# Optimization experiments

Measured on AMD Instinct MI355X. Metric: run time of the kernel, lower is better.

Reference implementation:

```python
import jax, jax.numpy as jnp
import numpy as np

NNZ = 16384
OUT_F = 1024
IN_F = 1024


def setup_inputs() -> dict:
    key = jax.random.key(0)
    k1, k2, k3, k4 = jax.random.split(key, 4)
    x = jax.random.normal(k1, (8, 4096, IN_F), dtype=jnp.float32)
    base_weight = (jax.random.normal(k2, (OUT_F, IN_F), dtype=jnp.float32) * 0.02).astype(jnp.float16)
    ortho_values = (jax.random.normal(k3, (NNZ,), dtype=jnp.float32) * 0.02).astype(jnp.float16)
    # unique flat indices (row * in_features + col), matching load_from_weights
    ortho_indices = jax.random.permutation(k4, OUT_F * IN_F)[:NNZ].astype(jnp.int32)
    alpha = jnp.ones((), dtype=jnp.float32)
    return {"x": x, "base_weight": base_weight, "ortho_values": ortho_values,
            "ortho_indices": ortho_indices, "alpha": alpha}


def reference(x, base_weight, ortho_values, ortho_indices, alpha):
    # Y = X @ W_base^T + alpha * (X @ W_ortho^T)  (torch F.linear convention)
    out_f, in_f = base_weight.shape
    lead = x.shape[:-1]
    xf = x.reshape(-1, in_f)  # [tokens, in]
    base_out = xf @ base_weight.astype(jnp.float32).T  # fp16 weight upcast, as in forward

    rows = ortho_indices // in_f
    cols = ortho_indices % in_f
    ortho_matrix = jnp.zeros((out_f, in_f), dtype=jnp.float32).at[rows, cols].set(
        ortho_values.astype(jnp.float32))
    ortho_out = xf @ ortho_matrix.T

    output = base_out + alpha.astype(jnp.float32) * ortho_out
    return output.reshape(*lead, out_f)
```

## Files before the change

kernel.cpp:

```cpp
#include <hip/hip_runtime.h>

#define IN_F 1024
#define OUT_F 1024
#define NNZ 16384

typedef _Float16 f16;
typedef _Float16 f16x4 __attribute__((ext_vector_type(4)));
typedef _Float16 f16x8 __attribute__((ext_vector_type(8)));
typedef float f32x4 __attribute__((ext_vector_type(4)));
typedef unsigned short ushort8 __attribute__((ext_vector_type(8)));

#define AS1 __attribute__((address_space(1)))
#define AS3 __attribute__((address_space(3)))


__device__ __forceinline__ int compute_mode(const unsigned short* __restrict__ w,
                                            float* smax, int* semax) {
  int t = threadIdx.x;
  const float* wf = (const float*)w;
  float m32 = fmaxf(fabsf(wf[t]), fabsf(wf[t + 256]));
  int e8 = 0;
#pragma unroll
  for (int j = 0; j < 8; ++j) {
    unsigned short u = w[t * 8 + j];
    int e = (u >> 7) & 0xFF;
    e8 = e > e8 ? e : e8;
  }
  smax[t] = m32; semax[t] = e8;
  __syncthreads();
  for (int s = 128; s > 0; s >>= 1) {
    if (t < s) {
      smax[t] = fmaxf(smax[t], smax[t + s]);
      semax[t] = semax[t] > semax[t + s] ? semax[t] : semax[t + s];
    }
    __syncthreads();
  }
  int m;
  if (!(smax[0] > 1e-6f)) m = 2;
  else if (semax[0] >= 140) m = 0;
  else m = 1;
  return m;
}

__device__ __forceinline__ float load_w(const void* base, size_t i, int mode) {
  if (mode == 0) return ((const float*)base)[i];
  if (mode == 1) {
    unsigned int u = (unsigned int)((const unsigned short*)base)[i] << 16;
    return __uint_as_float(u);
  }
  return (float)((const f16*)base)[i];
}

__global__ void prep_base(const void* __restrict__ base, f16* __restrict__ Wl) {
  __shared__ float smax[256];
  __shared__ int semax[256];
  int mode = compute_mode((const unsigned short*)base, smax, semax);
  int id = blockIdx.x * 256 + threadIdx.x;
  size_t off = (size_t)id * 8;
  f16x8 h;
  if (mode == 0) {
    const float* b = (const float*)base + off;
    float4 v0 = *reinterpret_cast<const float4*>(b);
    float4 v1 = *reinterpret_cast<const float4*>(b + 4);
    h = (f16x8){(f16)v0.x, (f16)v0.y, (f16)v0.z, (f16)v0.w,
                (f16)v1.x, (f16)v1.y, (f16)v1.z, (f16)v1.w};
  } else if (mode == 1) {
    ushort8 uv = *reinterpret_cast<const ushort8*>((const unsigned short*)base + off);
#pragma unroll
    for (int j = 0; j < 8; ++j)
      h[j] = (f16)__uint_as_float((unsigned int)uv[j] << 16);
  } else {
    h = *reinterpret_cast<const f16x8*>((const f16*)base + off);
  }
  *reinterpret_cast<f16x8*>(Wl + off) = h;
}

__global__ void prep_scatter(const void* __restrict__ base,
                             const void* __restrict__ vals,
                             const int* __restrict__ idx,
                             const float* __restrict__ alpha,
                             f16* __restrict__ Wl) {
  __shared__ float smax[256];
  __shared__ int semax[256];
  int mode = compute_mode((const unsigned short*)base, smax, semax);
  int i = blockIdx.x * 256 + threadIdx.x;
  if (i >= NNZ) return;
  int id = idx[i];
  float v = load_w(base, id, mode) + alpha[0] * load_w(vals, i, mode);
  Wl[id] = (f16)v;
}

__global__ void __launch_bounds__(256) conv_x(const float* __restrict__ X,
                                              f16* __restrict__ Xs, int total) {
  int stride = gridDim.x * 256;
  for (int id = blockIdx.x * 256 + threadIdx.x; id < total; id += stride) {
    size_t off = (size_t)id * 8;
    const float* p = X + off;
    float4 v0 = *reinterpret_cast<const float4*>(p);
    float4 v1 = *reinterpret_cast<const float4*>(p + 4);
    f16x8 h = {(f16)v0.x, (f16)v0.y, (f16)v0.z, (f16)v0.w,
               (f16)v1.x, (f16)v1.y, (f16)v1.z, (f16)v1.w};
    *reinterpret_cast<f16x8*>(Xs + off) = h;
  }
}

#define SB0 __builtin_amdgcn_sched_barrier(0)
#define VMW(N) asm volatile("s_waitcnt vmcnt(" #N ")" ::: "memory")


#define ISSUE_QA11(QI, KT1, AP)                                                \
    __builtin_amdgcn_global_load_lds(                                          \
        (const AS1 void*)(Xs + rowOffA[QI] + (KT1) * 64 + swzc),               \
        (AS3 void*)(&sA[((AP) * 4 + (QI)) * 4096 + t * 8]), 16, 0, 0)

#define ISSUE_QB11(QI, KT1, BP)                                                \
    __builtin_amdgcn_global_load_lds(                                          \
        (const AS1 void*)(Wl + rowOffB[QI] + (KT1) * 64 + swzc),               \
        (AS3 void*)(&sB[((BP) * 4 + (QI)) * 4096 + t * 8]), 16, 0, 0)

#define DSREAD11(AP, BP, S_) do {                                              \
    _Pragma("unroll")                                                          \
    for (int qq_ = 0; qq_ < 2; ++qq_) {                                        \
      int qa_ = ((AP) * 4 + wm * 2 + qq_) * 4096;                              \
      _Pragma("unroll")                                                        \
      for (int mf_ = 0; mf_ < 4; ++mf_) {                                      \
        int r_ = mf_ * 16 + lr;                                                \
        int blk_ = ((S_) * 4 + lk) ^ (lr & 7);                                 \
        afr[qq_][mf_] = *reinterpret_cast<const f16x8*>(&sA[qa_ + r_ * 64 + blk_ * 8]); \
      }                                                                        \
    }                                                                          \
    int qb_ = ((BP) * 4 + wn) * 4096;                                          \
    _Pragma("unroll")                                                          \
    for (int nf_ = 0; nf_ < 4; ++nf_) {                                        \
      int r_ = nf_ * 16 + lr;                                                  \
      int blk_ = ((S_) * 4 + lk) ^ (lr & 7);                                   \
      bfr[nf_] = *reinterpret_cast<const f16x8*>(&sB[qb_ + r_ * 64 + blk_ * 8]); \
    }                                                                          \
  } while (0)

#define MFMA32_FREE do {                                                       \
    __builtin_amdgcn_s_setprio(1);                                             \
    _Pragma("unroll")                                                          \
    for (int qq_ = 0; qq_ < 2; ++qq_)                                          \
      _Pragma("unroll")                                                        \
      for (int mf_ = 0; mf_ < 4; ++mf_)                                        \
        _Pragma("unroll")                                                      \
        for (int nf_ = 0; nf_ < 4; ++nf_)                                      \
          acc[qq_ * 4 + mf_][nf_] = __builtin_amdgcn_mfma_f32_16x16x32_f16(    \
              afr[qq_][mf_], bfr[nf_], acc[qq_ * 4 + mf_][nf_], 0, 0, 0);      \
    __builtin_amdgcn_s_setprio(0);                                             \
  } while (0)

#define KTILE12(AP, BP, KT, ISSB, ISSA, VMN, LASTBAR) do {                     \
    DSREAD11(AP, BP, 0);                                                       \
    if (ISSB) {                                                                \
      ISSUE_QB11(0, (KT) + 1, ((KT) + 1) & 1); ISSUE_QB11(1, (KT) + 1, ((KT) + 1) & 1); \
      ISSUE_QB11(2, (KT) + 1, ((KT) + 1) & 1); ISSUE_QB11(3, (KT) + 1, ((KT) + 1) & 1); } \
    MFMA32_FREE;                                                               \
    DSREAD11(AP, BP, 1);                                                       \
    if (ISSA) {                                                                \
      ISSUE_QA11(0, (KT) + 2, ((KT) + 2) % 3); ISSUE_QA11(1, (KT) + 2, ((KT) + 2) % 3); \
      ISSUE_QA11(2, (KT) + 2, ((KT) + 2) % 3); ISSUE_QA11(3, (KT) + 2, ((KT) + 2) % 3); } \
    MFMA32_FREE;                                                               \
    if (LASTBAR) {                                                             \
      VMW(VMN);                                                                \
      __builtin_amdgcn_s_barrier();             \
      SB0;                              \
    }                                                                          \
  } while (0)

__global__ void __launch_bounds__(512, 2) gemm12(const f16* __restrict__ Xs,
                                                 const f16* __restrict__ Wl,
                                                 float* __restrict__ C) {
  extern __shared__ f16 lds[];
  f16* sA = lds;
  f16* sB = lds + 49152;

  int bidx = blockIdx.x;
  int q = gridDim.x >> 3;
  int wg = (bidx & 7) * q + (bidx >> 3);
  int mt = wg >> 2, nt = wg & 3;

  int t = threadIdx.x;
  int lane = t & 63;
  int w = t >> 6;
  int wm = w >> 2;
  int wn = w & 3;
  int lr = lane & 15;
  int lk = lane >> 4;

  int rS = t >> 3;
  int swzc = (((t & 7) ^ (rS & 7)) << 3);
  size_t rowOffA[4], rowOffB[4];
#pragma unroll
  for (int qi = 0; qi < 4; ++qi) {
    rowOffA[qi] = (size_t)(mt * 256 + qi * 64 + rS) * IN_F;
    rowOffB[qi] = (size_t)(nt * 256 + qi * 64 + rS) * IN_F;
  }

  f16x8 afr[2][4], bfr[4];
  f32x4 acc[8][4];
#pragma unroll
  for (int i = 0; i < 8; ++i)
#pragma unroll
    for (int j = 0; j < 4; ++j)
      acc[i][j] = (f32x4){0.f, 0.f, 0.f, 0.f};

  ISSUE_QA11(0, 0, 0); ISSUE_QA11(1, 0, 0); ISSUE_QA11(2, 0, 0); ISSUE_QA11(3, 0, 0);
  ISSUE_QB11(0, 0, 0); ISSUE_QB11(1, 0, 0); ISSUE_QB11(2, 0, 0); ISSUE_QB11(3, 0, 0);
  ISSUE_QA11(0, 1, 1); ISSUE_QA11(1, 1, 1); ISSUE_QA11(2, 1, 1); ISSUE_QA11(3, 1, 1);
  VMW(4);
  __builtin_amdgcn_s_barrier();
  SB0;

  KTILE12(0, 0,  0, true,  true,  4, true);
  KTILE12(1, 1,  1, true,  true,  4, true);
  KTILE12(2, 0,  2, true,  true,  4, true);
  KTILE12(0, 1,  3, true,  true,  4, true);
  KTILE12(1, 0,  4, true,  true,  4, true);
  KTILE12(2, 1,  5, true,  true,  4, true);
  KTILE12(0, 0,  6, true,  true,  4, true);
  KTILE12(1, 1,  7, true,  true,  4, true);
  KTILE12(2, 0,  8, true,  true,  4, true);
  KTILE12(0, 1,  9, true,  true,  4, true);
  KTILE12(1, 0, 10, true,  true,  4, true);
  KTILE12(2, 1, 11, true,  true,  4, true);
  KTILE12(0, 0, 12, true,  true,  4, true);
  KTILE12(1, 1, 13, true,  true,  4, true);
  KTILE12(2, 0, 14, true,  false, 0, true);
  KTILE12(0, 1, 15, false, false, 0, false);

  float* Cw = C + (size_t)(mt * 256 + wm * 128 + lk * 4) * OUT_F + nt * 256 + wn * 64 + lr;
#pragma unroll
  for (int m = 0; m < 8; ++m) {
    int rowo = (m >> 2) * 64 + (m & 3) * 16;
#pragma unroll
    for (int nf = 0; nf < 4; ++nf)
#pragma unroll
      for (int g = 0; g < 4; ++g)
        Cw[(size_t)(rowo + g) * OUT_F + nf * 16] = acc[m][nf][g];
  }
}


#define MFMA32_PIN do {                                                        \
    asm volatile("s_waitcnt lgkmcnt(0)" ::: "memory");                         \
    SB0;                                                                       \
    __builtin_amdgcn_s_setprio(1);                                             \
    _Pragma("unroll")                                                          \
    for (int qq_ = 0; qq_ < 2; ++qq_)                                          \
      _Pragma("unroll")                                                        \
      for (int mf_ = 0; mf_ < 4; ++mf_)                                        \
        _Pragma("unroll")                                                      \
        for (int nf_ = 0; nf_ < 4; ++nf_)                                      \
          acc[qq_ * 4 + mf_][nf_] = __builtin_amdgcn_mfma_f32_16x16x32_f16(    \
              afr[qq_][mf_], bfr[nf_], acc[qq_ * 4 + mf_][nf_], 0, 0, 0);      \
    __builtin_amdgcn_s_setprio(0);                                             \
  } while (0)

#define KTILE11(AP, BP, KT, ISSB, ISSA, VMN, LASTBAR) do {                     \
    DSREAD11(AP, BP, 0);                                                       \
    if (ISSB) { SB0;                                                           \
      ISSUE_QB11(0, (KT) + 1, ((KT) + 1) & 1); ISSUE_QB11(1, (KT) + 1, ((KT) + 1) & 1); \
      ISSUE_QB11(2, (KT) + 1, ((KT) + 1) & 1); ISSUE_QB11(3, (KT) + 1, ((KT) + 1) & 1); } \
    MFMA32_PIN;                                                                \
    DSREAD11(AP, BP, 1);                                                       \
    if (ISSA) { SB0;                                                           \
      ISSUE_QA11(0, (KT) + 2, ((KT) + 2) % 3); ISSUE_QA11(1, (KT) + 2, ((KT) + 2) % 3); \
      ISSUE_QA11(2, (KT) + 2, ((KT) + 2) % 3); ISSUE_QA11(3, (KT) + 2, ((KT) + 2) % 3); } \
    MFMA32_PIN;                                                                \
    if (LASTBAR) {                                                             \
      SB0; VMW(VMN); SB0;                                                      \
      __builtin_amdgcn_s_barrier();                                            \
      SB0;                                                                     \
    }                                                                          \
  } while (0)

__global__ void __launch_bounds__(512, 2) gemm11(const f16* __restrict__ Xs,
                                                 const f16* __restrict__ Wl,
                                                 float* __restrict__ C) {
  extern __shared__ f16 lds[];
  f16* sA = lds;
  f16* sB = lds + 49152;

  int bidx = blockIdx.x;
  int q = gridDim.x >> 3;
  int wg = (bidx & 7) * q + (bidx >> 3);
  int mt = wg >> 2, nt = wg & 3;

  int t = threadIdx.x;
  int lane = t & 63;
  int w = t >> 6;
  int wm = w >> 2;
  int wn = w & 3;
  int lr = lane & 15;
  int lk = lane >> 4;

  int rS = t >> 3;
  int swzc = (((t & 7) ^ (rS & 7)) << 3);
  size_t rowOffA[4], rowOffB[4];
#pragma unroll
  for (int qi = 0; qi < 4; ++qi) {
    rowOffA[qi] = (size_t)(mt * 256 + qi * 64 + rS) * IN_F;
    rowOffB[qi] = (size_t)(nt * 256 + qi * 64 + rS) * IN_F;
  }

  f16x8 afr[2][4], bfr[4];
  f32x4 acc[8][4];
#pragma unroll
  for (int i = 0; i < 8; ++i)
#pragma unroll
    for (int j = 0; j < 4; ++j)
      acc[i][j] = (f32x4){0.f, 0.f, 0.f, 0.f};

  ISSUE_QA11(0, 0, 0); ISSUE_QA11(1, 0, 0); ISSUE_QA11(2, 0, 0); ISSUE_QA11(3, 0, 0);
  ISSUE_QB11(0, 0, 0); ISSUE_QB11(1, 0, 0); ISSUE_QB11(2, 0, 0); ISSUE_QB11(3, 0, 0);
  ISSUE_QA11(0, 1, 1); ISSUE_QA11(1, 1, 1); ISSUE_QA11(2, 1, 1); ISSUE_QA11(3, 1, 1);
  SB0; VMW(4); SB0;
  __builtin_amdgcn_s_barrier();
  SB0;

  KTILE11(0, 0,  0, true,  true,  4, true);
  KTILE11(1, 1,  1, true,  true,  4, true);
  KTILE11(2, 0,  2, true,  true,  4, true);
  KTILE11(0, 1,  3, true,  true,  4, true);
  KTILE11(1, 0,  4, true,  true,  4, true);
  KTILE11(2, 1,  5, true,  true,  4, true);
  KTILE11(0, 0,  6, true,  true,  4, true);
  KTILE11(1, 1,  7, true,  true,  4, true);
  KTILE11(2, 0,  8, true,  true,  4, true);
  KTILE11(0, 1,  9, true,  true,  4, true);
  KTILE11(1, 0, 10, true,  true,  4, true);
  KTILE11(2, 1, 11, true,  true,  4, true);
  KTILE11(0, 0, 12, true,  true,  4, true);
  KTILE11(1, 1, 13, true,  true,  4, true);
  KTILE11(2, 0, 14, true,  false, 0, true);
  KTILE11(0, 1, 15, false, false, 0, false);

  float* Cw = C + (size_t)(mt * 256 + wm * 128 + lk * 4) * OUT_F + nt * 256 + wn * 64 + lr;
#pragma unroll
  for (int m = 0; m < 8; ++m) {
    int rowo = (m >> 2) * 64 + (m & 3) * 16;
#pragma unroll
    for (int nf = 0; nf < 4; ++nf)
#pragma unroll
      for (int g = 0; g < 4; ++g)
        Cw[(size_t)(rowo + g) * OUT_F + nf * 16] = acc[m][nf][g];
  }
}

extern "C" void kernel_launch(void* const* d_in, const int* in_sizes, int n_in,
                              void* d_out, int out_size, void* d_ws, size_t ws_size,
                              hipStream_t stream) {
  const float* X = (const float*)d_in[0];
  const void* base = d_in[1];
  const void* vals = d_in[2];
  const int* idx = (const int*)d_in[3];
  const float* alpha = (const float*)d_in[4];
  float* out = (float*)d_out;
  f16* Wl = (f16*)d_ws;
  f16* Xs = (f16*)((char*)d_ws + 2 * 1024 * 1024 + 4096);

  int M = in_sizes[0] / IN_F;
  int total = (M * IN_F) / 8;

  prep_base<<<dim3(512), dim3(256), 0, stream>>>(base, Wl);
  prep_scatter<<<dim3((NNZ + 255) / 256), dim3(256), 0, stream>>>(base, vals, idx, alpha, Wl);
  conv_x<<<dim3(2048), dim3(256), 0, stream>>>(X, Xs, total);

  hipError_t e = hipFuncSetAttribute(reinterpret_cast<const void*>(&gemm12),
                                     hipFuncAttributeMaxDynamicSharedMemorySize, 163840);
  if (e == hipSuccess) {
    gemm12<<<dim3((M / 256) * 4), dim3(512), 163840, stream>>>(Xs, Wl, out);
  } else {
    (void)hipFuncSetAttribute(reinterpret_cast<const void*>(&gemm11),
                              hipFuncAttributeMaxDynamicSharedMemorySize, 163840);
    gemm11<<<dim3((M / 256) * 4), dim3(512), 163840, stream>>>(Xs, Wl, out);
  }
}
```

Baseline: 121.7 us.

## Switch GEMM to 128x128 tiles with 256 threads and fuse scatter into conv_x

Adds a new gemm13 kernel that uses 128x128 output tiles, 4 waves and half the LDS (80KB), launching four times as many workgroups. It keeps the same triple-buffered A and double-buffered B global_load_lds pipeline. The sparse scatter is also folded into the conv_x kernel, run by its first 64 blocks, which removes one launch. Smaller tiles give more blocks and better occupancy, but each tile reuses loaded data less and needs more global/L2 traffic. The scatter writing Wl inside conv_x, before gemm, stays ordered because it writes only Wl and runs after prep_base.

```diff
diff --git a/kernel.cpp b/kernel.cpp
--- a/kernel.cpp
+++ b/kernel.cpp
@@ -5,7 +5,6 @@
 #define NNZ 16384
 
 typedef _Float16 f16;
-typedef _Float16 f16x4 __attribute__((ext_vector_type(4)));
 typedef _Float16 f16x8 __attribute__((ext_vector_type(8)));
 typedef float f32x4 __attribute__((ext_vector_type(4)));
 typedef unsigned short ushort8 __attribute__((ext_vector_type(8)));
@@ -75,23 +74,22 @@
   *reinterpret_cast<f16x8*>(Wl + off) = h;
 }
 
-__global__ void prep_scatter(const void* __restrict__ base,
-                             const void* __restrict__ vals,
-                             const int* __restrict__ idx,
-                             const float* __restrict__ alpha,
-                             f16* __restrict__ Wl) {
+__global__ void __launch_bounds__(256) conv_x(const float* __restrict__ X,
+                                              f16* __restrict__ Xs, int total,
+                                              const void* __restrict__ base,
+                                              const void* __restrict__ vals,
+                                              const int* __restrict__ idx,
+                                              const float* __restrict__ alpha,
+                                              f16* __restrict__ Wl) {
   __shared__ float smax[256];
   __shared__ int semax[256];
-  int mode = compute_mode((const unsigned short*)base, smax, semax);
-  int i = blockIdx.x * 256 + threadIdx.x;
-  if (i >= NNZ) return;
-  int id = idx[i];
-  float v = load_w(base, id, mode) + alpha[0] * load_w(vals, i, mode);
-  Wl[id] = (f16)v;
-}
-
-__global__ void __launch_bounds__(256) conv_x(const float* __restrict__ X,
-                                              f16* __restrict__ Xs, int total) {
+  if (blockIdx.x < 64) {
+    int mode = compute_mode((const unsigned short*)base, smax, semax);
+    int i = blockIdx.x * 256 + threadIdx.x;
+    int id = idx[i];
+    float v = load_w(base, id, mode) + alpha[0] * load_w(vals, i, mode);
+    Wl[id] = (f16)v;
+  }
   int stride = gridDim.x * 256;
   for (int id = blockIdx.x * 256 + threadIdx.x; id < total; id += stride) {
     size_t off = (size_t)id * 8;
@@ -106,6 +104,142 @@
 
 #define SB0 __builtin_amdgcn_sched_barrier(0)
 #define VMW(N) asm volatile("s_waitcnt vmcnt(" #N ")" ::: "memory")
+
+
+#define ISSUE_QA13(QI, KT1, AP) do {                                           \
+    __builtin_amdgcn_global_load_lds(                                          \
+        (const AS1 void*)(Xs + rowOffA[QI][0] + (KT1) * 64 + swzc),            \
+        (AS3 void*)(&sA[((AP) * 2 + (QI)) * 4096 + t * 8]), 16, 0, 0);         \
+    __builtin_amdgcn_global_load_lds(                                          \
+        (const AS1 void*)(Xs + rowOffA[QI][1] + (KT1) * 64 + swzc),            \
+        (AS3 void*)(&sA[((AP) * 2 + (QI)) * 4096 + t * 8 + 2048]), 16, 0, 0);  \
+  } while (0)
+
+#define ISSUE_QB13(QI, KT1, BP) do {                                           \
+    __builtin_amdgcn_global_load_lds(                                          \
+        (const AS1 void*)(Wl + rowOffB[QI][0] + (KT1) * 64 + swzc),            \
+        (AS3 void*)(&sB[((BP) * 2 + (QI)) * 4096 + t * 8]), 16, 0, 0);         \
+    __builtin_amdgcn_global_load_lds(                                          \
+        (const AS1 void*)(Wl + rowOffB[QI][1] + (KT1) * 64 + swzc),            \
+        (AS3 void*)(&sB[((BP) * 2 + (QI)) * 4096 + t * 8 + 2048]), 16, 0, 0);  \
+  } while (0)
+
+#define DSREAD13(AP, BP, S_) do {                                              \
+    int qa_ = ((AP) * 2 + wm) * 4096;                                          \
+    _Pragma("unroll")                                                          \
+    for (int mf_ = 0; mf_ < 4; ++mf_) {                                        \
+      int r_ = mf_ * 16 + lr;                                                  \
+      int blk_ = ((S_) * 4 + lk) ^ (lr & 7);                                   \
+      afr[mf_] = *reinterpret_cast<const f16x8*>(&sA[qa_ + r_ * 64 + blk_ * 8]); \
+    }                                                                          \
+    int qb_ = ((BP) * 2 + wn) * 4096;                                          \
+    _Pragma("unroll")                                                          \
+    for (int nf_ = 0; nf_ < 4; ++nf_) {                                        \
+      int r_ = nf_ * 16 + lr;                                                  \
+      int blk_ = ((S_) * 4 + lk) ^ (lr & 7);                                   \
+      bfr[nf_] = *reinterpret_cast<const f16x8*>(&sB[qb_ + r_ * 64 + blk_ * 8]); \
+    }                                                                          \
+  } while (0)
+
+#define MFMA16F do {                                                           \
+    __builtin_amdgcn_s_setprio(1);                                             \
+    _Pragma("unroll")                                                          \
+    for (int mf_ = 0; mf_ < 4; ++mf_)                                          \
+      _Pragma("unroll")                                                        \
+      for (int nf_ = 0; nf_ < 4; ++nf_)                                        \
+        acc[mf_][nf_] = __builtin_amdgcn_mfma_f32_16x16x32_f16(                \
+            afr[mf_], bfr[nf_], acc[mf_][nf_], 0, 0, 0);                       \
+    __builtin_amdgcn_s_setprio(0);                                             \
+  } while (0)
+
+#define KTILE13(AP, BP, KT, ISSB, ISSA, VMN, LASTBAR) do {                     \
+    DSREAD13(AP, BP, 0);                                                       \
+    if (ISSB) { ISSUE_QB13(0, (KT) + 1, ((KT) + 1) & 1);                       \
+                ISSUE_QB13(1, (KT) + 1, ((KT) + 1) & 1); }                     \
+    MFMA16F;                                                                   \
+    DSREAD13(AP, BP, 1);                                                       \
+    if (ISSA) { ISSUE_QA13(0, (KT) + 2, ((KT) + 2) % 3);                       \
+                ISSUE_QA13(1, (KT) + 2, ((KT) + 2) % 3); }                     \
+    MFMA16F;                                                                   \
+    if (LASTBAR) {                                                             \
+      VMW(VMN);                                                                \
+      __builtin_amdgcn_s_barrier();             \
+      SB0;                                                    \
+    }                                                                          \
+  } while (0)
+
+__global__ void __launch_bounds__(256, 2) gemm13(const f16* __restrict__ Xs,
+                                                 const f16* __restrict__ Wl,
+                                                 float* __restrict__ C) {
+  extern __shared__ f16 lds[];
+  f16* sA = lds;
+  f16* sB = lds + 24576;
+
+  int bidx = blockIdx.x;
+  int q = gridDim.x >> 3;
+  int wg = (bidx & 7) * q + (bidx >> 3);
+  int mt = wg >> 3, nt = wg & 7;
+
+  int t = threadIdx.x;
+  int lane = t & 63;
+  int w = t >> 6;
+  int wm = w >> 1;
+  int wn = w & 1;
+  int lr = lane & 15;
+  int lk = lane >> 4;
+
+  int rS = t >> 3;
+  int swzc = (((t & 7) ^ (rS & 7)) << 3);
+  size_t rowOffA[2][2], rowOffB[2][2];
+#pragma unroll
+  for (int qi = 0; qi < 2; ++qi)
+#pragma unroll
+    for (int h = 0; h < 2; ++h) {
+      rowOffA[qi][h] = (size_t)(mt * 128 + qi * 64 + h * 32 + rS) * IN_F;
+      rowOffB[qi][h] = (size_t)(nt * 128 + qi * 64 + h * 32 + rS) * IN_F;
+    }
+
+  f16x8 afr[4], bfr[4];
+  f32x4 acc[4][4];
+#pragma unroll
+  for (int i = 0; i < 4; ++i)
+#pragma unroll
+    for (int j = 0; j < 4; ++j)
+      acc[i][j] = (f32x4){0.f, 0.f, 0.f, 0.f};
+
+  ISSUE_QA13(0, 0, 0); ISSUE_QA13(1, 0, 0);
+  ISSUE_QB13(0, 0, 0); ISSUE_QB13(1, 0, 0);
+  ISSUE_QA13(0, 1, 1); ISSUE_QA13(1, 1, 1);
+  VMW(4);
+  __builtin_amdgcn_s_barrier();
+  SB0;
+
+  KTILE13(0, 0,  0, true,  true,  4, true);
+  KTILE13(1, 1,  1, true,  true,  4, true);
+  KTILE13(2, 0,  2, true,  true,  4, true);
+  KTILE13(0, 1,  3, true,  true,  4, true);
+  KTILE13(1, 0,  4, true,  true,  4, true);
+  KTILE13(2, 1,  5, true,  true,  4, true);
+  KTILE13(0, 0,  6, true,  true,  4, true);
+  KTILE13(1, 1,  7, true,  true,  4, true);
+  KTILE13(2, 0,  8, true,  true,  4, true);
+  KTILE13(0, 1,  9, true,  true,  4, true);
+  KTILE13(1, 0, 10, true,  true,  4, true);
+  KTILE13(2, 1, 11, true,  true,  4, true);
+  KTILE13(0, 0, 12, true,  true,  4, true);
+  KTILE13(1, 1, 13, true,  true,  4, true);
+  KTILE13(2, 0, 14, true,  false, 0, true);
+  KTILE13(0, 1, 15, false, false, 0, false);
+
+  float* Cw = C + (size_t)(mt * 128 + wm * 64 + lk * 4) * OUT_F + nt * 128 + wn * 64 + lr;
+#pragma unroll
+  for (int mf = 0; mf < 4; ++mf)
+#pragma unroll
+    for (int nf = 0; nf < 4; ++nf)
+#pragma unroll
+      for (int g = 0; g < 4; ++g)
+        Cw[(size_t)(mf * 16 + g) * OUT_F + nf * 16] = acc[mf][nf][g];
+}
 
 
 #define ISSUE_QA11(QI, KT1, AP)                                                \
@@ -164,8 +298,8 @@
     MFMA32_FREE;                                                               \
     if (LASTBAR) {                                                             \
       VMW(VMN);                                                                \
-      __builtin_amdgcn_s_barrier();             \
-      SB0;                              \
+      __builtin_amdgcn_s_barrier();                                            \
+      SB0;                                                                     \
     }                                                                          \
   } while (0)
 
@@ -242,113 +376,6 @@
   }
 }
 
-
-#define MFMA32_PIN do {                                                        \
-    asm volatile("s_waitcnt lgkmcnt(0)" ::: "memory");                         \
-    SB0;                                                                       \
-    __builtin_amdgcn_s_setprio(1);                                             \
-    _Pragma("unroll")                                                          \
-    for (int qq_ = 0; qq_ < 2; ++qq_)                                          \
-      _Pragma("unroll")                                                        \
-      for (int mf_ = 0; mf_ < 4; ++mf_)                                        \
-        _Pragma("unroll")                                                      \
-        for (int nf_ = 0; nf_ < 4; ++nf_)                                      \
-          acc[qq_ * 4 + mf_][nf_] = __builtin_amdgcn_mfma_f32_16x16x32_f16(    \
-              afr[qq_][mf_], bfr[nf_], acc[qq_ * 4 + mf_][nf_], 0, 0, 0);      \
-    __builtin_amdgcn_s_setprio(0);                                             \
-  } while (0)
-
-#define KTILE11(AP, BP, KT, ISSB, ISSA, VMN, LASTBAR) do {                     \
-    DSREAD11(AP, BP, 0);                                                       \
-    if (ISSB) { SB0;                                                           \
-      ISSUE_QB11(0, (KT) + 1, ((KT) + 1) & 1); ISSUE_QB11(1, (KT) + 1, ((KT) + 1) & 1); \
-      ISSUE_QB11(2, (KT) + 1, ((KT) + 1) & 1); ISSUE_QB11(3, (KT) + 1, ((KT) + 1) & 1); } \
-    MFMA32_PIN;                                                                \
-    DSREAD11(AP, BP, 1);                                                       \
-    if (ISSA) { SB0;                                                           \
-      ISSUE_QA11(0, (KT) + 2, ((KT) + 2) % 3); ISSUE_QA11(1, (KT) + 2, ((KT) + 2) % 3); \
-      ISSUE_QA11(2, (KT) + 2, ((KT) + 2) % 3); ISSUE_QA11(3, (KT) + 2, ((KT) + 2) % 3); } \
-    MFMA32_PIN;                                                                \
-    if (LASTBAR) {                                                             \
-      SB0; VMW(VMN); SB0;                                                      \
-      __builtin_amdgcn_s_barrier();                                            \
-      SB0;                                                                     \
-    }                                                                          \
-  } while (0)
-
-__global__ void __launch_bounds__(512, 2) gemm11(const f16* __restrict__ Xs,
-                                                 const f16* __restrict__ Wl,
-                                                 float* __restrict__ C) {
-  extern __shared__ f16 lds[];
-  f16* sA = lds;
-  f16* sB = lds + 49152;
-
-  int bidx = blockIdx.x;
-  int q = gridDim.x >> 3;
-  int wg = (bidx & 7) * q + (bidx >> 3);
-  int mt = wg >> 2, nt = wg & 3;
-
-  int t = threadIdx.x;
-  int lane = t & 63;
-  int w = t >> 6;
-  int wm = w >> 2;
-  int wn = w & 3;
-  int lr = lane & 15;
-  int lk = lane >> 4;
-
-  int rS = t >> 3;
-  int swzc = (((t & 7) ^ (rS & 7)) << 3);
-  size_t rowOffA[4], rowOffB[4];
-#pragma unroll
-  for (int qi = 0; qi < 4; ++qi) {
-    rowOffA[qi] = (size_t)(mt * 256 + qi * 64 + rS) * IN_F;
-    rowOffB[qi] = (size_t)(nt * 256 + qi * 64 + rS) * IN_F;
-  }
-
-  f16x8 afr[2][4], bfr[4];
-  f32x4 acc[8][4];
-#pragma unroll
-  for (int i = 0; i < 8; ++i)
-#pragma unroll
-    for (int j = 0; j < 4; ++j)
-      acc[i][j] = (f32x4){0.f, 0.f, 0.f, 0.f};
-
-  ISSUE_QA11(0, 0, 0); ISSUE_QA11(1, 0, 0); ISSUE_QA11(2, 0, 0); ISSUE_QA11(3, 0, 0);
-  ISSUE_QB11(0, 0, 0); ISSUE_QB11(1, 0, 0); ISSUE_QB11(2, 0, 0); ISSUE_QB11(3, 0, 0);
-  ISSUE_QA11(0, 1, 1); ISSUE_QA11(1, 1, 1); ISSUE_QA11(2, 1, 1); ISSUE_QA11(3, 1, 1);
-  SB0; VMW(4); SB0;
-  __builtin_amdgcn_s_barrier();
-  SB0;
-
-  KTILE11(0, 0,  0, true,  true,  4, true);
-  KTILE11(1, 1,  1, true,  true,  4, true);
-  KTILE11(2, 0,  2, true,  true,  4, true);
-  KTILE11(0, 1,  3, true,  true,  4, true);
-  KTILE11(1, 0,  4, true,  true,  4, true);
-  KTILE11(2, 1,  5, true,  true,  4, true);
-  KTILE11(0, 0,  6, true,  true,  4, true);
-  KTILE11(1, 1,  7, true,  true,  4, true);
-  KTILE11(2, 0,  8, true,  true,  4, true);
-  KTILE11(0, 1,  9, true,  true,  4, true);
-  KTILE11(1, 0, 10, true,  true,  4, true);
-  KTILE11(2, 1, 11, true,  true,  4, true);
-  KTILE11(0, 0, 12, true,  true,  4, true);
-  KTILE11(1, 1, 13, true,  true,  4, true);
-  KTILE11(2, 0, 14, true,  false, 0, true);
-  KTILE11(0, 1, 15, false, false, 0, false);
-
-  float* Cw = C + (size_t)(mt * 256 + wm * 128 + lk * 4) * OUT_F + nt * 256 + wn * 64 + lr;
-#pragma unroll
-  for (int m = 0; m < 8; ++m) {
-    int rowo = (m >> 2) * 64 + (m & 3) * 16;
-#pragma unroll
-    for (int nf = 0; nf < 4; ++nf)
-#pragma unroll
-      for (int g = 0; g < 4; ++g)
-        Cw[(size_t)(rowo + g) * OUT_F + nf * 16] = acc[m][nf][g];
-  }
-}
-
 extern "C" void kernel_launch(void* const* d_in, const int* in_sizes, int n_in,
                               void* d_out, int out_size, void* d_ws, size_t ws_size,
                               hipStream_t stream) {
@@ -365,16 +392,15 @@
   int total = (M * IN_F) / 8;
 
   prep_base<<<dim3(512), dim3(256), 0, stream>>>(base, Wl);
-  prep_scatter<<<dim3((NNZ + 255) / 256), dim3(256), 0, stream>>>(base, vals, idx, alpha, Wl);
-  conv_x<<<dim3(2048), dim3(256), 0, stream>>>(X, Xs, total);
-
-  hipError_t e = hipFuncSetAttribute(reinterpret_cast<const void*>(&gemm12),
-                                     hipFuncAttributeMaxDynamicSharedMemorySize, 163840);
+  conv_x<<<dim3(2048), dim3(256), 0, stream>>>(X, Xs, total, base, vals, idx, alpha, Wl);
+
+  hipError_t e = hipFuncSetAttribute(reinterpret_cast<const void*>(&gemm13),
+                                     hipFuncAttributeMaxDynamicSharedMemorySize, 81920);
   if (e == hipSuccess) {
+    gemm13<<<dim3((M / 128) * 8), dim3(256), 81920, stream>>>(Xs, Wl, out);
+  } else {
+    (void)hipFuncSetAttribute(reinterpret_cast<const void*>(&gemm12),
+                              hipFuncAttributeMaxDynamicSharedMemorySize, 163840);
     gemm12<<<dim3((M / 256) * 4), dim3(512), 163840, stream>>>(Xs, Wl, out);
-  } else {
-    (void)hipFuncSetAttribute(reinterpret_cast<const void*>(&gemm11),
-                              hipFuncAttributeMaxDynamicSharedMemorySize, 163840);
-    gemm11<<<dim3((M / 256) * 4), dim3(512), 163840, stream>>>(Xs, Wl, out);
-  }
-}
+  }
+}
```

Result: faster. 119.1 us (-2.1%).

## Fuse fp32-to-fp16 X conversion into GEMM by staging fp32 tiles in LDS

Applied to the files above, without the earlier changes.

The separate conv_x pass that converts X to fp16 is removed. A new gemm14 kernel streams fp32 X directly into LDS in half-width K tiles and converts to fp16 while building fragments. B tiles are reloaded every other step, with a reworked wait/barrier schedule. This avoids writing and re-reading a 64 MB fp16 copy of X, at the cost of twice the LDS traffic for A, per-fragment conversion ALU work, and twice as many barriers.

```diff
diff --git a/kernel.cpp b/kernel.cpp
--- a/kernel.cpp
+++ b/kernel.cpp
@@ -5,7 +5,6 @@
 #define NNZ 16384
 
 typedef _Float16 f16;
-typedef _Float16 f16x4 __attribute__((ext_vector_type(4)));
 typedef _Float16 f16x8 __attribute__((ext_vector_type(8)));
 typedef float f32x4 __attribute__((ext_vector_type(4)));
 typedef unsigned short ushort8 __attribute__((ext_vector_type(8)));
@@ -108,6 +107,169 @@
 #define VMW(N) asm volatile("s_waitcnt vmcnt(" #N ")" ::: "memory")
 
 
+#define ISSUE_A14(QI, KT1, AP)                                                 \
+    __builtin_amdgcn_global_load_lds(                                          \
+        (const AS1 void*)(X + rowOffA[QI] + (KT1) * 32 + swzcA),               \
+        (AS3 void*)(&sAf[((AP) * 4 + (QI)) * 2048 + t * 4]), 16, 0, 0)
+
+#define ISSUE_B14(QI, KTB1, BP)                                                \
+    __builtin_amdgcn_global_load_lds(                                          \
+        (const AS1 void*)(Wl + rowOffB[QI] + (KTB1) * 64 + swzc),              \
+        (AS3 void*)(&sB[((BP) * 4 + (QI)) * 4096 + t * 8]), 16, 0, 0)
+
+#define DSREAD_A14(AP) do {                                                    \
+    _Pragma("unroll")                                                          \
+    for (int qq_ = 0; qq_ < 2; ++qq_) {                                        \
+      int qa_ = ((AP) * 4 + wm * 2 + qq_) * 2048;                              \
+      _Pragma("unroll")                                                        \
+      for (int mf_ = 0; mf_ < 4; ++mf_) {                                      \
+        int r_ = mf_ * 16 + lr;                                                \
+        f32x4 a0_ = *reinterpret_cast<const f32x4*>(                           \
+            &sAf[qa_ + r_ * 32 + (((2 * lk) ^ (r_ & 7)) << 2)]);               \
+        f32x4 a1_ = *reinterpret_cast<const f32x4*>(                           \
+            &sAf[qa_ + r_ * 32 + (((2 * lk + 1) ^ (r_ & 7)) << 2)]);           \
+        afr[qq_][mf_] = (f16x8){(f16)a0_[0], (f16)a0_[1], (f16)a0_[2],         \
+                                (f16)a0_[3], (f16)a1_[0], (f16)a1_[1],         \
+                                (f16)a1_[2], (f16)a1_[3]};                     \
+      }                                                                        \
+    }                                                                          \
+  } while (0)
+
+#define DSREAD_B14(BP, S_) do {                                                \
+    int qb_ = ((BP) * 4 + wn) * 4096;                                          \
+    _Pragma("unroll")                                                          \
+    for (int nf_ = 0; nf_ < 4; ++nf_) {                                        \
+      int r_ = nf_ * 16 + lr;                                                  \
+      int blk_ = ((S_) * 4 + lk) ^ (lr & 7);                                   \
+      bfr[nf_] = *reinterpret_cast<const f16x8*>(&sB[qb_ + r_ * 64 + blk_ * 8]); \
+    }                                                                          \
+  } while (0)
+
+#define MFMA32_14 do {                                                         \
+    __builtin_amdgcn_s_setprio(1);                                             \
+    _Pragma("unroll")                                                          \
+    for (int qq_ = 0; qq_ < 2; ++qq_)                                          \
+      _Pragma("unroll")                                                        \
+      for (int mf_ = 0; mf_ < 4; ++mf_)                                        \
+        _Pragma("unroll")                                                      \
+        for (int nf_ = 0; nf_ < 4; ++nf_)                                      \
+          acc[qq_ * 4 + mf_][nf_] = __builtin_amdgcn_mfma_f32_16x16x32_f16(    \
+              afr[qq_][mf_], bfr[nf_], acc[qq_ * 4 + mf_][nf_], 0, 0, 0);      \
+    __builtin_amdgcn_s_setprio(0);                                             \
+  } while (0)
+
+#define KTILE14(AP, BP, S_, KT, ISSB, ISSA, VMN, GATE) do {                    \
+    DSREAD_A14(AP);                                                            \
+    DSREAD_B14(BP, S_);                                                        \
+    if (ISSB) {                                                                \
+      ISSUE_B14(0, ((KT) >> 1) + 1, (((KT) >> 1) + 1) & 1);                    \
+      ISSUE_B14(1, ((KT) >> 1) + 1, (((KT) >> 1) + 1) & 1);                    \
+      ISSUE_B14(2, ((KT) >> 1) + 1, (((KT) >> 1) + 1) & 1);                    \
+      ISSUE_B14(3, ((KT) >> 1) + 1, (((KT) >> 1) + 1) & 1); }                  \
+    MFMA32_14;                                                                 \
+    if (ISSA) {                                                                \
+      ISSUE_A14(0, (KT) + 2, ((KT) + 2) % 3);                                  \
+      ISSUE_A14(1, (KT) + 2, ((KT) + 2) % 3);                                  \
+      ISSUE_A14(2, (KT) + 2, ((KT) + 2) % 3);                                  \
+      ISSUE_A14(3, (KT) + 2, ((KT) + 2) % 3); }                                \
+    if (GATE) {                                                                \
+      VMW(VMN);                                                                \
+      __builtin_amdgcn_s_barrier();             \
+      SB0;                                                    \
+    }                                                                          \
+  } while (0)
+
+__global__ void __launch_bounds__(512, 2) gemm14(const float* __restrict__ X,
+                                                 const f16* __restrict__ Wl,
+                                                 float* __restrict__ C) {
+  extern __shared__ char lds[];
+  float* sAf = (float*)lds;
+  f16* sB = (f16*)(lds + 98304);
+
+  int bidx = blockIdx.x;
+  int q = gridDim.x >> 3;
+  int wg = (bidx & 7) * q + (bidx >> 3);
+  int mt = wg >> 2, nt = wg & 3;
+
+  int t = threadIdx.x;
+  int lane = t & 63;
+  int w = t >> 6;
+  int wm = w >> 2;
+  int wn = w & 3;
+  int lr = lane & 15;
+  int lk = lane >> 4;
+
+  int rS = t >> 3;
+  int swzc = (((t & 7) ^ (rS & 7)) << 3);
+  int swzcA = (((t & 7) ^ (rS & 7)) << 2);
+  size_t rowOffA[4], rowOffB[4];
+#pragma unroll
+  for (int qi = 0; qi < 4; ++qi) {
+    rowOffA[qi] = (size_t)(mt * 256 + qi * 64 + rS) * IN_F;
+    rowOffB[qi] = (size_t)(nt * 256 + qi * 64 + rS) * IN_F;
+  }
+
+  f16x8 afr[2][4], bfr[4];
+  f32x4 acc[8][4];
+#pragma unroll
+  for (int i = 0; i < 8; ++i)
+#pragma unroll
+    for (int j = 0; j < 4; ++j)
+      acc[i][j] = (f32x4){0.f, 0.f, 0.f, 0.f};
+
+  ISSUE_A14(0, 0, 0); ISSUE_A14(1, 0, 0); ISSUE_A14(2, 0, 0); ISSUE_A14(3, 0, 0);
+  ISSUE_B14(0, 0, 0); ISSUE_B14(1, 0, 0); ISSUE_B14(2, 0, 0); ISSUE_B14(3, 0, 0);
+  ISSUE_A14(0, 1, 1); ISSUE_A14(1, 1, 1); ISSUE_A14(2, 1, 1); ISSUE_A14(3, 1, 1);
+  VMW(4);
+  __builtin_amdgcn_s_barrier();
+  SB0;
+
+  KTILE14(0, 0, 0,  0, true,  true,  8, true);
+  KTILE14(1, 0, 1,  1, false, true,  4, true);
+  KTILE14(2, 1, 0,  2, true,  true,  8, true);
+  KTILE14(0, 1, 1,  3, false, true,  4, true);
+  KTILE14(1, 0, 0,  4, true,  true,  8, true);
+  KTILE14(2, 0, 1,  5, false, true,  4, true);
+  KTILE14(0, 1, 0,  6, true,  true,  8, true);
+  KTILE14(1, 1, 1,  7, false, true,  4, true);
+  KTILE14(2, 0, 0,  8, true,  true,  8, true);
+  KTILE14(0, 0, 1,  9, false, true,  4, true);
+  KTILE14(1, 1, 0, 10, true,  true,  8, true);
+  KTILE14(2, 1, 1, 11, false, true,  4, true);
+  KTILE14(0, 0, 0, 12, true,  true,  8, true);
+  KTILE14(1, 0, 1, 13, false, true,  4, true);
+  KTILE14(2, 1, 0, 14, true,  true,  8, true);
+  KTILE14(0, 1, 1, 15, false, true,  4, true);
+  KTILE14(1, 0, 0, 16, true,  true,  8, true);
+  KTILE14(2, 0, 1, 17, false, true,  4, true);
+  KTILE14(0, 1, 0, 18, true,  true,  8, true);
+  KTILE14(1, 1, 1, 19, false, true,  4, true);
+  KTILE14(2, 0, 0, 20, true,  true,  8, true);
+  KTILE14(0, 0, 1, 21, false, true,  4, true);
+  KTILE14(1, 1, 0, 22, true,  true,  8, true);
+  KTILE14(2, 1, 1, 23, false, true,  4, true);
+  KTILE14(0, 0, 0, 24, true,  true,  8, true);
+  KTILE14(1, 0, 1, 25, false, true,  4, true);
+  KTILE14(2, 1, 0, 26, true,  true,  8, true);
+  KTILE14(0, 1, 1, 27, false, true,  4, true);
+  KTILE14(1, 0, 0, 28, true,  true,  8, true);
+  KTILE14(2, 0, 1, 29, false, true,  4, true);
+  KTILE14(0, 1, 0, 30, false, false, 0, true);
+  KTILE14(1, 1, 1, 31, false, false, 0, false);
+
+  float* Cw = C + (size_t)(mt * 256 + wm * 128 + lk * 4) * OUT_F + nt * 256 + wn * 64 + lr;
+#pragma unroll
+  for (int m = 0; m < 8; ++m) {
+    int rowo = (m >> 2) * 64 + (m & 3) * 16;
+#pragma unroll
+    for (int nf = 0; nf < 4; ++nf)
+#pragma unroll
+      for (int g = 0; g < 4; ++g)
+        Cw[(size_t)(rowo + g) * OUT_F + nf * 16] = acc[m][nf][g];
+  }
+}
+
+
 #define ISSUE_QA11(QI, KT1, AP)                                                \
     __builtin_amdgcn_global_load_lds(                                          \
         (const AS1 void*)(Xs + rowOffA[QI] + (KT1) * 64 + swzc),               \
@@ -138,43 +300,30 @@
     }                                                                          \
   } while (0)
 
-#define MFMA32_FREE do {                                                       \
-    __builtin_amdgcn_s_setprio(1);                                             \
-    _Pragma("unroll")                                                          \
-    for (int qq_ = 0; qq_ < 2; ++qq_)                                          \
-      _Pragma("unroll")                                                        \
-      for (int mf_ = 0; mf_ < 4; ++mf_)                                        \
-        _Pragma("unroll")                                                      \
-        for (int nf_ = 0; nf_ < 4; ++nf_)                                      \
-          acc[qq_ * 4 + mf_][nf_] = __builtin_amdgcn_mfma_f32_16x16x32_f16(    \
-              afr[qq_][mf_], bfr[nf_], acc[qq_ * 4 + mf_][nf_], 0, 0, 0);      \
-    __builtin_amdgcn_s_setprio(0);                                             \
-  } while (0)
-
 #define KTILE12(AP, BP, KT, ISSB, ISSA, VMN, LASTBAR) do {                     \
     DSREAD11(AP, BP, 0);                                                       \
     if (ISSB) {                                                                \
       ISSUE_QB11(0, (KT) + 1, ((KT) + 1) & 1); ISSUE_QB11(1, (KT) + 1, ((KT) + 1) & 1); \
       ISSUE_QB11(2, (KT) + 1, ((KT) + 1) & 1); ISSUE_QB11(3, (KT) + 1, ((KT) + 1) & 1); } \
-    MFMA32_FREE;                                                               \
+    MFMA32_14;                                                                 \
     DSREAD11(AP, BP, 1);                                                       \
     if (ISSA) {                                                                \
       ISSUE_QA11(0, (KT) + 2, ((KT) + 2) % 3); ISSUE_QA11(1, (KT) + 2, ((KT) + 2) % 3); \
       ISSUE_QA11(2, (KT) + 2, ((KT) + 2) % 3); ISSUE_QA11(3, (KT) + 2, ((KT) + 2) % 3); } \
-    MFMA32_FREE;                                                               \
+    MFMA32_14;                                                                 \
     if (LASTBAR) {                                                             \
       VMW(VMN);                                                                \
-      __builtin_amdgcn_s_barrier();             \
-      SB0;                              \
+      __builtin_amdgcn_s_barrier();                                            \
+      SB0;                                                                     \
     }                                                                          \
   } while (0)
 
 __global__ void __launch_bounds__(512, 2) gemm12(const f16* __restrict__ Xs,
                                                  const f16* __restrict__ Wl,
                                                  float* __restrict__ C) {
-  extern __shared__ f16 lds[];
-  f16* sA = lds;
-  f16* sB = lds + 49152;
+  extern __shared__ char lds[];
+  f16* sA = (f16*)lds;
+  f16* sB = (f16*)(lds + 98304);
 
   int bidx = blockIdx.x;
   int q = gridDim.x >> 3;
@@ -242,113 +391,6 @@
   }
 }
 
-
-#define MFMA32_PIN do {                                                        \
-    asm volatile("s_waitcnt lgkmcnt(0)" ::: "memory");                         \
-    SB0;                                                                       \
-    __builtin_amdgcn_s_setprio(1);                                             \
-    _Pragma("unroll")                                                          \
-    for (int qq_ = 0; qq_ < 2; ++qq_)                                          \
-      _Pragma("unroll")                                                        \
-      for (int mf_ = 0; mf_ < 4; ++mf_)                                        \
-        _Pragma("unroll")                                                      \
-        for (int nf_ = 0; nf_ < 4; ++nf_)                                      \
-          acc[qq_ * 4 + mf_][nf_] = __builtin_amdgcn_mfma_f32_16x16x32_f16(    \
-              afr[qq_][mf_], bfr[nf_], acc[qq_ * 4 + mf_][nf_], 0, 0, 0);      \
-    __builtin_amdgcn_s_setprio(0);                                             \
-  } while (0)
-
-#define KTILE11(AP, BP, KT, ISSB, ISSA, VMN, LASTBAR) do {                     \
-    DSREAD11(AP, BP, 0);                                                       \
-    if (ISSB) { SB0;                                                           \
-      ISSUE_QB11(0, (KT) + 1, ((KT) + 1) & 1); ISSUE_QB11(1, (KT) + 1, ((KT) + 1) & 1); \
-      ISSUE_QB11(2, (KT) + 1, ((KT) + 1) & 1); ISSUE_QB11(3, (KT) + 1, ((KT) + 1) & 1); } \
-    MFMA32_PIN;                                                                \
-    DSREAD11(AP, BP, 1);                                                       \
-    if (ISSA) { SB0;                                                           \
-      ISSUE_QA11(0, (KT) + 2, ((KT) + 2) % 3); ISSUE_QA11(1, (KT) + 2, ((KT) + 2) % 3); \
-      ISSUE_QA11(2, (KT) + 2, ((KT) + 2) % 3); ISSUE_QA11(3, (KT) + 2, ((KT) + 2) % 3); } \
-    MFMA32_PIN;                                                                \
-    if (LASTBAR) {                                                             \
-      SB0; VMW(VMN); SB0;                                                      \
-      __builtin_amdgcn_s_barrier();                                            \
-      SB0;                                                                     \
-    }                                                                          \
-  } while (0)
-
-__global__ void __launch_bounds__(512, 2) gemm11(const f16* __restrict__ Xs,
-                                                 const f16* __restrict__ Wl,
-                                                 float* __restrict__ C) {
-  extern __shared__ f16 lds[];
-  f16* sA = lds;
-  f16* sB = lds + 49152;
-
-  int bidx = blockIdx.x;
-  int q = gridDim.x >> 3;
-  int wg = (bidx & 7) * q + (bidx >> 3);
-  int mt = wg >> 2, nt = wg & 3;
-
-  int t = threadIdx.x;
-  int lane = t & 63;
-  int w = t >> 6;
-  int wm = w >> 2;
-  int wn = w & 3;
-  int lr = lane & 15;
-  int lk = lane >> 4;
-
-  int rS = t >> 3;
-  int swzc = (((t & 7) ^ (rS & 7)) << 3);
-  size_t rowOffA[4], rowOffB[4];
-#pragma unroll
-  for (int qi = 0; qi < 4; ++qi) {
-    rowOffA[qi] = (size_t)(mt * 256 + qi * 64 + rS) * IN_F;
-    rowOffB[qi] = (size_t)(nt * 256 + qi * 64 + rS) * IN_F;
-  }
-
-  f16x8 afr[2][4], bfr[4];
-  f32x4 acc[8][4];
-#pragma unroll
-  for (int i = 0; i < 8; ++i)
-#pragma unroll
-    for (int j = 0; j < 4; ++j)
-      acc[i][j] = (f32x4){0.f, 0.f, 0.f, 0.f};
-
-  ISSUE_QA11(0, 0, 0); ISSUE_QA11(1, 0, 0); ISSUE_QA11(2, 0, 0); ISSUE_QA11(3, 0, 0);
-  ISSUE_QB11(0, 0, 0); ISSUE_QB11(1, 0, 0); ISSUE_QB11(2, 0, 0); ISSUE_QB11(3, 0, 0);
-  ISSUE_QA11(0, 1, 1); ISSUE_QA11(1, 1, 1); ISSUE_QA11(2, 1, 1); ISSUE_QA11(3, 1, 1);
-  SB0; VMW(4); SB0;
-  __builtin_amdgcn_s_barrier();
-  SB0;
-
-  KTILE11(0, 0,  0, true,  true,  4, true);
-  KTILE11(1, 1,  1, true,  true,  4, true);
-  KTILE11(2, 0,  2, true,  true,  4, true);
-  KTILE11(0, 1,  3, true,  true,  4, true);
-  KTILE11(1, 0,  4, true,  true,  4, true);
-  KTILE11(2, 1,  5, true,  true,  4, true);
-  KTILE11(0, 0,  6, true,  true,  4, true);
-  KTILE11(1, 1,  7, true,  true,  4, true);
-  KTILE11(2, 0,  8, true,  true,  4, true);
-  KTILE11(0, 1,  9, true,  true,  4, true);
-  KTILE11(1, 0, 10, true,  true,  4, true);
-  KTILE11(2, 1, 11, true,  true,  4, true);
-  KTILE11(0, 0, 12, true,  true,  4, true);
-  KTILE11(1, 1, 13, true,  true,  4, true);
-  KTILE11(2, 0, 14, true,  false, 0, true);
-  KTILE11(0, 1, 15, false, false, 0, false);
-
-  float* Cw = C + (size_t)(mt * 256 + wm * 128 + lk * 4) * OUT_F + nt * 256 + wn * 64 + lr;
-#pragma unroll
-  for (int m = 0; m < 8; ++m) {
-    int rowo = (m >> 2) * 64 + (m & 3) * 16;
-#pragma unroll
-    for (int nf = 0; nf < 4; ++nf)
-#pragma unroll
-      for (int g = 0; g < 4; ++g)
-        Cw[(size_t)(rowo + g) * OUT_F + nf * 16] = acc[m][nf][g];
-  }
-}
-
 extern "C" void kernel_launch(void* const* d_in, const int* in_sizes, int n_in,
                               void* d_out, int out_size, void* d_ws, size_t ws_size,
                               hipStream_t stream) {
@@ -365,16 +407,16 @@
   int total = (M * IN_F) / 8;
 
   prep_base<<<dim3(512), dim3(256), 0, stream>>>(base, Wl);
-  prep_scatter<<<dim3((NNZ + 255) / 256), dim3(256), 0, stream>>>(base, vals, idx, alpha, Wl);
-  conv_x<<<dim3(2048), dim3(256), 0, stream>>>(X, Xs, total);
-
-  hipError_t e = hipFuncSetAttribute(reinterpret_cast<const void*>(&gemm12),
+  prep_scatter<<<dim3(64), dim3(256), 0, stream>>>(base, vals, idx, alpha, Wl);
+
+  hipError_t e = hipFuncSetAttribute(reinterpret_cast<const void*>(&gemm14),
                                      hipFuncAttributeMaxDynamicSharedMemorySize, 163840);
   if (e == hipSuccess) {
+    gemm14<<<dim3((M / 256) * 4), dim3(512), 163840, stream>>>(X, Wl, out);
+  } else {
+    (void)hipFuncSetAttribute(reinterpret_cast<const void*>(&gemm12),
+                              hipFuncAttributeMaxDynamicSharedMemorySize, 163840);
+    conv_x<<<dim3(2048), dim3(256), 0, stream>>>(X, Xs, total);
     gemm12<<<dim3((M / 256) * 4), dim3(512), 163840, stream>>>(Xs, Wl, out);
-  } else {
-    (void)hipFuncSetAttribute(reinterpret_cast<const void*>(&gemm11),
-                              hipFuncAttributeMaxDynamicSharedMemorySize, 163840);
-    gemm11<<<dim3((M / 256) * 4), dim3(512), 163840, stream>>>(Xs, Wl, out);
-  }
-}
+  }
+}
```

New measurement: 104.9 us, median of 2. -13.8%, faster.
